# Kernel optimization log

Measured on AMD Instinct MI355X. Metric: run time of the kernel, lower is better.

Reference implementation:

```python
import jax, jax.numpy as jnp
import numpy as np

B, S, D = 4, 2048, 1024
D_K, D_V = 1024, 1024


def setup_inputs() -> dict:
    key = jax.random.key(0)
    ks = jax.random.split(key, 9)
    s = 1.0 / np.sqrt(D)
    return {
        "q_in": jax.random.normal(ks[0], (B, S, D), jnp.float32),
        "k_in": jax.random.normal(ks[1], (B, S, D), jnp.float32),
        "v_in": jax.random.normal(ks[2], (B, S, D), jnp.float32),
        "Wq": jax.random.normal(ks[3], (D, D_K), jnp.float32) * s,
        "bq": jnp.zeros((D_K,), jnp.float32),
        "Wk": jax.random.normal(ks[4], (D, D_K), jnp.float32) * s,
        "bk": jnp.zeros((D_K,), jnp.float32),
        "Wv": jax.random.normal(ks[5], (D, D_V), jnp.float32) * s,
        "bv": jnp.zeros((D_V,), jnp.float32),
    }


def reference(q_in, k_in, v_in, Wq, bq, Wk, bk, Wv, bv):
    q = jnp.einsum("bsd,dk->bsk", q_in, Wq) + bq  # [B,S,d_k]
    k = jnp.einsum("bsd,dk->bsk", k_in, Wk) + bk  # [B,S,d_k]
    v = jnp.einsum("bsd,dv->bsv", v_in, Wv) + bv  # [B,S,d_v]
    scores = jnp.einsum("bqk,bsk->bqs", q, k) / jnp.sqrt(jnp.float32(D_K))
    attn = jax.nn.softmax(scores, axis=-1)  # [B,S,S]
    return jnp.einsum("bqs,bsv->bqv", attn, v)
```

## Files before the change

kernel.cpp:

```cpp
#include <hip/hip_runtime.h>
#include <stdint.h>

#define B_  4
#define S_  2048
#define D_  1024
#define DK_ 1024
#define DV_ 1024

typedef __attribute__((ext_vector_type(8)))  short short8;
typedef __attribute__((ext_vector_type(16))) float floatx16;

#define ASYNC16(gsrc, ldst)                                                        \
  __builtin_amdgcn_global_load_lds(                                                \
      (const __attribute__((address_space(1))) unsigned int*)(gsrc),               \
      (__attribute__((address_space(3))) unsigned int*)(ldst), 16, 0, 0)

__device__ __forceinline__ unsigned short f2bf(float f) {
  union { float f; uint32_t u; } v; v.f = f;
  uint32_t r = v.u + 0x7fffu + ((v.u >> 16) & 1u);
  return (unsigned short)(r >> 16);
}
__device__ __forceinline__ float bf2f(unsigned short h) {
  union { float f; uint32_t u; } v; v.u = ((uint32_t)h) << 16;
  return v.f;
}

__global__ __launch_bounds__(256) void cvt3_f32_bf16(const float* __restrict__ a,
                                                     const float* __restrict__ b,
                                                     const float* __restrict__ c,
                                                     unsigned short* __restrict__ out, int n4) {
  const float* in = (blockIdx.z == 0) ? a : (blockIdx.z == 1) ? b : c;
  unsigned short* o = out + (long)blockIdx.z * n4 * 4;
  int i = blockIdx.x * 256 + threadIdx.x;
  if (i >= n4) return;
  float4 v = ((const float4*)in)[i];
  ushort4 u;
  u.x = f2bf(v.x); u.y = f2bf(v.y); u.z = f2bf(v.z); u.w = f2bf(v.w);
  ((ushort4*)o)[i] = u;
}

__global__ __launch_bounds__(256) void transpose3_f32_bf16(const float* __restrict__ W0,
                                                           const float* __restrict__ W1,
                                                           const float* __restrict__ W2,
                                                           unsigned short* __restrict__ out,
                                                           int rows, int cols) {
  const float* in = (blockIdx.z == 0) ? W0 : (blockIdx.z == 1) ? W1 : W2;
  unsigned short* o = out + (long)blockIdx.z * rows * cols;
  __shared__ float tile[32][33];
  int bx = blockIdx.x * 32, by = blockIdx.y * 32;
  int tx = threadIdx.x & 31, ty = threadIdx.x >> 5;
  for (int r = ty; r < 32; r += 8)
    tile[r][tx] = in[(long)(by + r) * cols + bx + tx];
  __syncthreads();
  for (int r = ty; r < 32; r += 8)
    o[(long)(bx + r) * rows + by + tx] = f2bf(tile[tx][r]);
}

__global__ __launch_bounds__(256) void transpose_bf16_batched(const unsigned short* __restrict__ in,
                                                              unsigned short* __restrict__ out,
                                                              int rows, int cols) {
  in  += (long)blockIdx.z * rows * cols;
  out += (long)blockIdx.z * rows * cols;
  __shared__ unsigned short tile[32][33];
  int bx = blockIdx.x * 32, by = blockIdx.y * 32;
  int tx = threadIdx.x & 31, ty = threadIdx.x >> 5;
  for (int r = ty; r < 32; r += 8)
    tile[r][tx] = in[(long)(by + r) * cols + bx + tx];
  __syncthreads();
  for (int r = ty; r < 32; r += 8)
    out[(long)(bx + r) * rows + by + tx] = tile[tx][r];
}

__device__ __forceinline__ void storeC(float* p, float v)          { *p = v; }
__device__ __forceinline__ void storeC(unsigned short* p, float v) { *p = f2bf(v); }

template <typename OutT, int NOUT>
__global__ __launch_bounds__(256)
void gemm_bt32(const unsigned short* __restrict__ A0, const unsigned short* __restrict__ A1,
               const unsigned short* __restrict__ A2, const unsigned short* __restrict__ Bm,
               OutT* __restrict__ C0, OutT* __restrict__ C1, OutT* __restrict__ C2,
               const float* __restrict__ b0, const float* __restrict__ b1,
               const float* __restrict__ b2,
               int N, int K, long sA, long sB, long sC, float scale) {
  __shared__ __align__(16) unsigned short As[2][128 * 32];
  __shared__ __align__(16) unsigned short Bs[2][128 * 32];
  const int tid  = threadIdx.x;
  const int lane = tid & 63, wave = tid >> 6;
  const int wm = (wave >> 1) * 64, wn = (wave & 1) * 64;
  const int lm = lane & 31;
  const int hi = lane >> 5;
  const long zb = blockIdx.z;
  const int m0  = blockIdx.y * 128;
  const int n0g = blockIdx.x * 128;

  const unsigned short* A = A0;
  OutT* C = C0;
  const float* bias = b0;
  int n0 = n0g;
  if (NOUT == 3) {
    int sel = n0g >> 10;
    n0 = n0g & 1023;
    if (sel == 1)      { A = A1; C = C1; bias = b1; }
    else if (sel == 2) { A = A2; C = C2; bias = b2; }
  }
  A += zb * sA;
  const unsigned short* Bp = Bm + zb * sB;
  C += zb * sC;

  const int rr = lane >> 2;
  const int cc = (((lane & 3) ^ ((lane >> 3) & 3)) * 8);
  const unsigned short* agA = A  + (long)(m0  + 16 * wave + rr) * K + cc;
  const unsigned short* agB = Bp + (long)(n0g + 16 * wave + rr) * K + cc;
  const unsigned short* ag0 = agA;
  const unsigned short* ag1 = agA + 32;
  const unsigned short* ag2 = agA + 64 * (long)K;
  const unsigned short* ag3 = agA + 64 * (long)K + 32;
  const unsigned short* bg0 = agB;
  const unsigned short* bg1 = agB + 32;
  const unsigned short* bg2 = agB + 64 * (long)K;
  const unsigned short* bg3 = agB + 64 * (long)K + 32;
  unsigned short* al0 = &As[0][wave * 512];
  unsigned short* al1 = &As[1][wave * 512];
  unsigned short* al2 = &As[0][(wave + 4) * 512];
  unsigned short* al3 = &As[1][(wave + 4) * 512];
  unsigned short* bl0 = &Bs[0][wave * 512];
  unsigned short* bl1 = &Bs[1][wave * 512];
  unsigned short* bl2 = &Bs[0][(wave + 4) * 512];
  unsigned short* bl3 = &Bs[1][(wave + 4) * 512];

  floatx16 acc[2][2] = {};
  const int sw = (lm >> 1) & 3;

  for (int kt = 0; kt < K; kt += 64) {
    __syncthreads();
    ASYNC16(ag0, al0); ASYNC16(ag1, al1); ASYNC16(ag2, al2); ASYNC16(ag3, al3);
    ASYNC16(bg0, bl0); ASYNC16(bg1, bl1); ASYNC16(bg2, bl2); ASYNC16(bg3, bl3);
    __syncthreads();

#pragma unroll
    for (int s = 0; s < 4; s++) {
      const int h   = s >> 1;
      const int off = (((s & 1) * 2 + hi) ^ sw) * 8;
      short8 af[2], bf[2];
#pragma unroll
      for (int i = 0; i < 2; i++)
        af[i] = *(const short8*)&As[h][(wm + i * 32 + lm) * 32 + off];
#pragma unroll
      for (int j = 0; j < 2; j++)
        bf[j] = *(const short8*)&Bs[h][(wn + j * 32 + lm) * 32 + off];
#pragma unroll
      for (int i = 0; i < 2; i++)
#pragma unroll
        for (int j = 0; j < 2; j++)
          acc[i][j] = __builtin_amdgcn_mfma_f32_32x32x16_bf16(af[i], bf[j], acc[i][j], 0, 0, 0);
    }
    ag0 += 64; ag1 += 64; ag2 += 64; ag3 += 64;
    bg0 += 64; bg1 += 64; bg2 += 64; bg3 += 64;
  }

#pragma unroll
  for (int i = 0; i < 2; i++) {
#pragma unroll
    for (int j = 0; j < 2; j++) {
      const int col = n0 + wn + j * 32 + lm;
      const float bv = bias ? bias[col] : 0.f;
#pragma unroll
      for (int r = 0; r < 16; r++) {
        const int row = m0 + wm + i * 32 + (r & 3) + ((r >> 2) << 3) + (hi << 2);
        storeC(C + (long)row * N + col, acc[i][j][r] * scale + bv);
      }
    }
  }
}

__global__ __launch_bounds__(256) void softmax_rows_bf16(const unsigned short* __restrict__ Sc,
                                                         unsigned short* __restrict__ P) {
  const long row = blockIdx.x;
  const int tid = threadIdx.x;
  short8 xv = ((const short8*)(Sc + row * 2048))[tid];
  float v[8];
  float m = -3.4e38f;
#pragma unroll
  for (int j = 0; j < 8; j++) { v[j] = bf2f((unsigned short)xv[j]); m = fmaxf(m, v[j]); }
#pragma unroll
  for (int off = 32; off > 0; off >>= 1) m = fmaxf(m, __shfl_xor(m, off, 64));
  __shared__ float redm[4], reds[4];
  if ((tid & 63) == 0) redm[tid >> 6] = m;
  __syncthreads();
  m = fmaxf(fmaxf(redm[0], redm[1]), fmaxf(redm[2], redm[3]));
  float s = 0.f;
#pragma unroll
  for (int j = 0; j < 8; j++) { v[j] = __expf(v[j] - m); s += v[j]; }
#pragma unroll
  for (int off = 32; off > 0; off >>= 1) s += __shfl_xor(s, off, 64);
  if ((tid & 63) == 0) reds[tid >> 6] = s;
  __syncthreads();
  s = reds[0] + reds[1] + reds[2] + reds[3];
  float inv = 1.f / s;
  short8 ov;
#pragma unroll
  for (int j = 0; j < 8; j++) ov[j] = (short)f2bf(v[j] * inv);
  ((short8*)(P + row * 2048))[tid] = ov;
}

extern "C" void kernel_launch(void* const* d_in, const int* in_sizes, int n_in,
                              void* d_out, int out_size, void* d_ws, size_t ws_size,
                              hipStream_t stream) {
  const float* q_in = (const float*)d_in[0];
  const float* k_in = (const float*)d_in[1];
  const float* v_in = (const float*)d_in[2];
  const float* Wq   = (const float*)d_in[3];
  const float* bq   = (const float*)d_in[4];
  const float* Wk   = (const float*)d_in[5];
  const float* bk   = (const float*)d_in[6];
  const float* Wv   = (const float*)d_in[7];
  const float* bv   = (const float*)d_in[8];
  float* out = (float*)d_out;

  char* ws = (char*)d_ws;
  const long nX = (long)B_ * S_ * D_;
  const long nW = (long)D_ * DK_;
  unsigned short* qb  = (unsigned short*)(ws);
  unsigned short* kb  = qb + nX;
  unsigned short* vb  = kb + nX;
  unsigned short* WqT = vb + nX;
  unsigned short* Vb  = WqT + 3 * nW;
  unsigned short* Qb  = Vb + nX;
  unsigned short* Kb  = Qb + nX;
  unsigned short* Vt  = Kb + nX;
  unsigned short* scoresB = (unsigned short*)ws;
  unsigned short* attn    = Vt + nX;

  dim3 blk(256);

  {
    int n4 = (int)(nX / 4);
    dim3 g(n4 / 256, 1, 3);
    cvt3_f32_bf16<<<g, blk, 0, stream>>>(q_in, k_in, v_in, qb, n4);
  }
  {
    dim3 g(DK_ / 32, D_ / 32, 3);
    transpose3_f32_bf16<<<g, blk, 0, stream>>>(Wq, Wk, Wv, WqT, D_, DK_);
  }
  {
    dim3 g(3 * DK_ / 128, (B_ * S_) / 128, 1);
    gemm_bt32<unsigned short, 3><<<g, blk, 0, stream>>>(
        qb, kb, vb, WqT, Qb, Kb, Vb, bq, bk, bv, DK_, D_, 0, 0, 0, 1.f);
  }
  {
    dim3 g(DV_ / 32, S_ / 32, B_);
    transpose_bf16_batched<<<g, blk, 0, stream>>>(Vb, Vt, S_, DV_);
  }
  {
    dim3 g(S_ / 128, S_ / 128, B_);
    gemm_bt32<unsigned short, 1><<<g, blk, 0, stream>>>(
        Qb, nullptr, nullptr, Kb, scoresB, nullptr, nullptr, nullptr, nullptr, nullptr,
        S_, DK_, (long)S_ * DK_, (long)S_ * DK_, (long)S_ * S_, 0.03125f);
  }
  {
    dim3 g(B_ * S_);
    softmax_rows_bf16<<<g, blk, 0, stream>>>(scoresB, attn);
  }
  {
    dim3 g(DV_ / 128, S_ / 128, B_);
    gemm_bt32<float, 1><<<g, blk, 0, stream>>>(
        attn, nullptr, nullptr, Vt, out, nullptr, nullptr, nullptr, nullptr, nullptr,
        DV_, S_, (long)S_ * S_, (long)DV_ * S_, (long)S_ * DV_, 1.f);
  }
}
```

Measured before the change: 354.5 us.

## Fuse softmax into QK and PV GEMM epilogues, fold V transpose and prep kernels

Removes the separate softmax kernel. The scores GEMM epilogue now writes unnormalized exp(scaled score) in bf16 and atomically accumulates per-row sums. The PV GEMM then scales its output rows by the reciprocal sum. The V projection epilogue writes V already transposed, which drops the transpose kernel, and the input cast and weight transpose are merged into one launch. Skipping max subtraction risks overflow for larger score magnitudes, and the atomics plus the extra memset add some cost.

```diff
diff --git a/kernel.cpp b/kernel.cpp
--- a/kernel.cpp
+++ b/kernel.cpp
@@ -20,70 +20,56 @@
   uint32_t r = v.u + 0x7fffu + ((v.u >> 16) & 1u);
   return (unsigned short)(r >> 16);
 }
-__device__ __forceinline__ float bf2f(unsigned short h) {
-  union { float f; uint32_t u; } v; v.u = ((uint32_t)h) << 16;
-  return v.f;
-}
-
-__global__ __launch_bounds__(256) void cvt3_f32_bf16(const float* __restrict__ a,
-                                                     const float* __restrict__ b,
-                                                     const float* __restrict__ c,
-                                                     unsigned short* __restrict__ out, int n4) {
-  const float* in = (blockIdx.z == 0) ? a : (blockIdx.z == 1) ? b : c;
-  unsigned short* o = out + (long)blockIdx.z * n4 * 4;
-  int i = blockIdx.x * 256 + threadIdx.x;
-  if (i >= n4) return;
-  float4 v = ((const float4*)in)[i];
-  ushort4 u;
-  u.x = f2bf(v.x); u.y = f2bf(v.y); u.z = f2bf(v.z); u.w = f2bf(v.w);
-  ((ushort4*)o)[i] = u;
-}
-
-__global__ __launch_bounds__(256) void transpose3_f32_bf16(const float* __restrict__ W0,
-                                                           const float* __restrict__ W1,
-                                                           const float* __restrict__ W2,
-                                                           unsigned short* __restrict__ out,
-                                                           int rows, int cols) {
-  const float* in = (blockIdx.z == 0) ? W0 : (blockIdx.z == 1) ? W1 : W2;
-  unsigned short* o = out + (long)blockIdx.z * rows * cols;
-  __shared__ float tile[32][33];
-  int bx = blockIdx.x * 32, by = blockIdx.y * 32;
-  int tx = threadIdx.x & 31, ty = threadIdx.x >> 5;
-  for (int r = ty; r < 32; r += 8)
-    tile[r][tx] = in[(long)(by + r) * cols + bx + tx];
-  __syncthreads();
-  for (int r = ty; r < 32; r += 8)
-    o[(long)(bx + r) * rows + by + tx] = f2bf(tile[tx][r]);
-}
-
-__global__ __launch_bounds__(256) void transpose_bf16_batched(const unsigned short* __restrict__ in,
-                                                              unsigned short* __restrict__ out,
-                                                              int rows, int cols) {
-  in  += (long)blockIdx.z * rows * cols;
-  out += (long)blockIdx.z * rows * cols;
-  __shared__ unsigned short tile[32][33];
-  int bx = blockIdx.x * 32, by = blockIdx.y * 32;
-  int tx = threadIdx.x & 31, ty = threadIdx.x >> 5;
-  for (int r = ty; r < 32; r += 8)
-    tile[r][tx] = in[(long)(by + r) * cols + bx + tx];
-  __syncthreads();
-  for (int r = ty; r < 32; r += 8)
-    out[(long)(bx + r) * rows + by + tx] = tile[tx][r];
+
+__global__ __launch_bounds__(256)
+void prep(const float* __restrict__ q, const float* __restrict__ k, const float* __restrict__ v,
+          const float* __restrict__ W0, const float* __restrict__ W1, const float* __restrict__ W2,
+          unsigned short* __restrict__ qkv, unsigned short* __restrict__ WT) {
+  const int bid = blockIdx.x, tid = threadIdx.x;
+  if (bid < 12288) {
+    const int t  = bid >> 12;
+    const int cb = bid & 4095;
+    const float* in = (t == 0) ? q : (t == 1) ? k : v;
+    unsigned short* o = qkv + (long)t * ((long)B_ * S_ * D_);
+    const int i0 = cb * 512 + tid;
+    float4 v0 = ((const float4*)in)[i0];
+    float4 v1 = ((const float4*)in)[i0 + 256];
+    ushort4 u0, u1;
+    u0.x = f2bf(v0.x); u0.y = f2bf(v0.y); u0.z = f2bf(v0.z); u0.w = f2bf(v0.w);
+    u1.x = f2bf(v1.x); u1.y = f2bf(v1.y); u1.z = f2bf(v1.z); u1.w = f2bf(v1.w);
+    ((ushort4*)o)[i0] = u0;
+    ((ushort4*)o)[i0 + 256] = u1;
+  } else {
+    const int b2 = bid - 12288;
+    const int w  = b2 >> 10;
+    const int tl = b2 & 1023;
+    const float* in = (w == 0) ? W0 : (w == 1) ? W1 : W2;
+    unsigned short* o = WT + (long)w * D_ * DK_;
+    __shared__ float tile[32][33];
+    const int bx = (tl & 31) * 32, by = (tl >> 5) * 32;
+    const int tx = tid & 31, ty = tid >> 5;
+    for (int r = ty; r < 32; r += 8)
+      tile[r][tx] = in[(long)(by + r) * DK_ + bx + tx];
+    __syncthreads();
+    for (int r = ty; r < 32; r += 8)
+      o[(long)(bx + r) * D_ + by + tx] = f2bf(tile[tx][r]);
+  }
 }
 
 __device__ __forceinline__ void storeC(float* p, float v)          { *p = v; }
 __device__ __forceinline__ void storeC(unsigned short* p, float v) { *p = f2bf(v); }
 
-template <typename OutT, int NOUT>
+template <typename OutT, int NOUT, int MODE>
 __global__ __launch_bounds__(256)
 void gemm_bt32(const unsigned short* __restrict__ A0, const unsigned short* __restrict__ A1,
                const unsigned short* __restrict__ A2, const unsigned short* __restrict__ Bm,
                OutT* __restrict__ C0, OutT* __restrict__ C1, OutT* __restrict__ C2,
                const float* __restrict__ b0, const float* __restrict__ b1,
-               const float* __restrict__ b2,
+               const float* __restrict__ b2, float* __restrict__ rowsum,
                int N, int K, long sA, long sB, long sC, float scale) {
   __shared__ __align__(16) unsigned short As[2][128 * 32];
   __shared__ __align__(16) unsigned short Bs[2][128 * 32];
+  __shared__ float invs[128];
   const int tid  = threadIdx.x;
   const int lane = tid & 63, wave = tid >> 6;
   const int wm = (wave >> 1) * 64, wn = (wave & 1) * 64;
@@ -96,9 +82,9 @@
   const unsigned short* A = A0;
   OutT* C = C0;
   const float* bias = b0;
-  int n0 = n0g;
+  int n0 = n0g, sel = 0;
   if (NOUT == 3) {
-    int sel = n0g >> 10;
+    sel = n0g >> 10;
     n0 = n0g & 1023;
     if (sel == 1)      { A = A1; C = C1; bias = b1; }
     else if (sel == 2) { A = A2; C = C2; bias = b2; }
@@ -158,49 +144,71 @@
     bg0 += 64; bg1 += 64; bg2 += 64; bg3 += 64;
   }
 
-#pragma unroll
-  for (int i = 0; i < 2; i++) {
-#pragma unroll
-    for (int j = 0; j < 2; j++) {
-      const int col = n0 + wn + j * 32 + lm;
-      const float bv = bias ? bias[col] : 0.f;
+  if (MODE == 2) {
+    __syncthreads();
+    if (tid < 128) invs[tid] = 1.0f / rowsum[zb * S_ + m0 + tid];
+    __syncthreads();
+  }
+
+  if (NOUT == 3 && sel == 2) {
+    unsigned short* Vt = (unsigned short*)C;
+    const int b = m0 >> 11;
+    const int sbase = (m0 & 2047);
+#pragma unroll
+    for (int i = 0; i < 2; i++) {
+      const int srowb = sbase + wm + i * 32 + (hi << 2);
+#pragma unroll
+      for (int j = 0; j < 2; j++) {
+        const int col = n0 + wn + j * 32 + lm;
+        const float bv = bias[col];
+        unsigned short* vp = Vt + ((long)b * DV_ + col) * S_ + srowb;
+#pragma unroll
+        for (int g = 0; g < 4; g++) {
+          ushort4 u;
+          u.x = f2bf(acc[i][j][4 * g + 0] + bv);
+          u.y = f2bf(acc[i][j][4 * g + 1] + bv);
+          u.z = f2bf(acc[i][j][4 * g + 2] + bv);
+          u.w = f2bf(acc[i][j][4 * g + 3] + bv);
+          *(ushort4*)(vp + 8 * g) = u;
+        }
+      }
+    }
+  } else if (MODE == 1) {
+#pragma unroll
+    for (int i = 0; i < 2; i++) {
 #pragma unroll
       for (int r = 0; r < 16; r++) {
         const int row = m0 + wm + i * 32 + (r & 3) + ((r >> 2) << 3) + (hi << 2);
-        storeC(C + (long)row * N + col, acc[i][j][r] * scale + bv);
+        float sum2 = 0.f;
+#pragma unroll
+        for (int j = 0; j < 2; j++) {
+          const int col = n0 + wn + j * 32 + lm;
+          float e = __expf(acc[i][j][r] * scale);
+          storeC(C + (long)row * N + col, e);
+          sum2 += e;
+        }
+#pragma unroll
+        for (int msk = 1; msk < 32; msk <<= 1) sum2 += __shfl_xor(sum2, msk, 64);
+        if ((lane & 31) == 0) atomicAdd(&rowsum[zb * S_ + row], sum2);
       }
     }
-  }
-}
-
-__global__ __launch_bounds__(256) void softmax_rows_bf16(const unsigned short* __restrict__ Sc,
-                                                         unsigned short* __restrict__ P) {
-  const long row = blockIdx.x;
-  const int tid = threadIdx.x;
-  short8 xv = ((const short8*)(Sc + row * 2048))[tid];
-  float v[8];
-  float m = -3.4e38f;
-#pragma unroll
-  for (int j = 0; j < 8; j++) { v[j] = bf2f((unsigned short)xv[j]); m = fmaxf(m, v[j]); }
-#pragma unroll
-  for (int off = 32; off > 0; off >>= 1) m = fmaxf(m, __shfl_xor(m, off, 64));
-  __shared__ float redm[4], reds[4];
-  if ((tid & 63) == 0) redm[tid >> 6] = m;
-  __syncthreads();
-  m = fmaxf(fmaxf(redm[0], redm[1]), fmaxf(redm[2], redm[3]));
-  float s = 0.f;
-#pragma unroll
-  for (int j = 0; j < 8; j++) { v[j] = __expf(v[j] - m); s += v[j]; }
-#pragma unroll
-  for (int off = 32; off > 0; off >>= 1) s += __shfl_xor(s, off, 64);
-  if ((tid & 63) == 0) reds[tid >> 6] = s;
-  __syncthreads();
-  s = reds[0] + reds[1] + reds[2] + reds[3];
-  float inv = 1.f / s;
-  short8 ov;
-#pragma unroll
-  for (int j = 0; j < 8; j++) ov[j] = (short)f2bf(v[j] * inv);
-  ((short8*)(P + row * 2048))[tid] = ov;
+  } else {
+#pragma unroll
+    for (int i = 0; i < 2; i++) {
+#pragma unroll
+      for (int j = 0; j < 2; j++) {
+        const int col = n0 + wn + j * 32 + lm;
+        const float bv = bias ? bias[col] : 0.f;
+#pragma unroll
+        for (int r = 0; r < 16; r++) {
+          const int rl = wm + i * 32 + (r & 3) + ((r >> 2) << 3) + (hi << 2);
+          float val = acc[i][j][r] * scale + bv;
+          if (MODE == 2) val *= invs[rl];
+          storeC(C + (long)(m0 + rl) * N + col, val);
+        }
+      }
+    }
+  }
 }
 
 extern "C" void kernel_launch(void* const* d_in, const int* in_sizes, int n_in,
@@ -224,47 +232,35 @@
   unsigned short* kb  = qb + nX;
   unsigned short* vb  = kb + nX;
   unsigned short* WqT = vb + nX;
-  unsigned short* Vb  = WqT + 3 * nW;
-  unsigned short* Qb  = Vb + nX;
+  unsigned short* Qb  = WqT + 3 * nW;
   unsigned short* Kb  = Qb + nX;
   unsigned short* Vt  = Kb + nX;
-  unsigned short* scoresB = (unsigned short*)ws;
-  unsigned short* attn    = Vt + nX;
+  float*          rowsum = (float*)(Vt + nX);
+  unsigned short* U   = (unsigned short*)ws;
 
   dim3 blk(256);
 
-  {
-    int n4 = (int)(nX / 4);
-    dim3 g(n4 / 256, 1, 3);
-    cvt3_f32_bf16<<<g, blk, 0, stream>>>(q_in, k_in, v_in, qb, n4);
-  }
-  {
-    dim3 g(DK_ / 32, D_ / 32, 3);
-    transpose3_f32_bf16<<<g, blk, 0, stream>>>(Wq, Wk, Wv, WqT, D_, DK_);
+  hipMemsetAsync(rowsum, 0, (size_t)B_ * S_ * sizeof(float), stream);
+
+  {
+    dim3 g(12288 + 3072);
+    prep<<<g, blk, 0, stream>>>(q_in, k_in, v_in, Wq, Wk, Wv, qb, WqT);
   }
   {
     dim3 g(3 * DK_ / 128, (B_ * S_) / 128, 1);
-    gemm_bt32<unsigned short, 3><<<g, blk, 0, stream>>>(
-        qb, kb, vb, WqT, Qb, Kb, Vb, bq, bk, bv, DK_, D_, 0, 0, 0, 1.f);
-  }
-  {
-    dim3 g(DV_ / 32, S_ / 32, B_);
-    transpose_bf16_batched<<<g, blk, 0, stream>>>(Vb, Vt, S_, DV_);
+    gemm_bt32<unsigned short, 3, 0><<<g, blk, 0, stream>>>(
+        qb, kb, vb, WqT, Qb, Kb, Vt, bq, bk, bv, nullptr, DK_, D_, 0, 0, 0, 1.f);
   }
   {
     dim3 g(S_ / 128, S_ / 128, B_);
-    gemm_bt32<unsigned short, 1><<<g, blk, 0, stream>>>(
-        Qb, nullptr, nullptr, Kb, scoresB, nullptr, nullptr, nullptr, nullptr, nullptr,
+    gemm_bt32<unsigned short, 1, 1><<<g, blk, 0, stream>>>(
+        Qb, nullptr, nullptr, Kb, U, nullptr, nullptr, nullptr, nullptr, nullptr, rowsum,
         S_, DK_, (long)S_ * DK_, (long)S_ * DK_, (long)S_ * S_, 0.03125f);
   }
   {
-    dim3 g(B_ * S_);
-    softmax_rows_bf16<<<g, blk, 0, stream>>>(scoresB, attn);
-  }
-  {
     dim3 g(DV_ / 128, S_ / 128, B_);
-    gemm_bt32<float, 1><<<g, blk, 0, stream>>>(
-        attn, nullptr, nullptr, Vt, out, nullptr, nullptr, nullptr, nullptr, nullptr,
+    gemm_bt32<float, 1, 2><<<g, blk, 0, stream>>>(
+        U, nullptr, nullptr, Vt, out, nullptr, nullptr, nullptr, nullptr, nullptr, rowsum,
         DV_, S_, (long)S_ * S_, (long)DV_ * S_, (long)S_ * DV_, 1.f);
   }
 }
```

Result: faster. 344.1 us (-2.9%).
